# Performance work log

Hardware: AMD Instinct MI355X
Metric: run time of the kernel (lower is better)

## Reference

```python
import jax, jax.numpy as jnp
import numpy as np

N_NODES = 50000
N_EDGES = 800000
NODE_IN = 5
EDGE_IN = 1
HID = 64


def setup_inputs() -> dict:
    key = jax.random.key(0)
    ks = jax.random.split(key, 16)
    x = jax.random.normal(ks[0], (N_NODES, NODE_IN), dtype=jnp.float32)
    edge_index = jax.random.randint(ks[1], (2, N_EDGES), 0, N_NODES, dtype=jnp.int32)
    edge_attr = jax.random.normal(ks[2], (N_EDGES, EDGE_IN), dtype=jnp.float32)
    def lin(k, fan_in, fan_out):
        b = 1.0 / np.sqrt(fan_in)
        k1, k2 = jax.random.split(k)
        W = jax.random.uniform(k1, (fan_in, fan_out), minval=-b, maxval=b, dtype=jnp.float32)
        bi = jax.random.uniform(k2, (fan_out,), minval=-b, maxval=b, dtype=jnp.float32)
        return W, bi
    W_ne, b_ne = lin(ks[3], NODE_IN, HID)
    W_ee, b_ee = lin(ks[4], EDGE_IN, HID)
    W_gcn, b_gcn = lin(ks[5], HID, HID)   # PyG GCNConv: lin (no bias) + separate bias
    W1, b1 = lin(ks[6], 3 * HID, HID)
    W2, b2 = lin(ks[7], HID, 1)
    return {"x": x, "edge_index": edge_index, "edge_attr": edge_attr,
            "W_ne": W_ne, "b_ne": b_ne, "W_ee": W_ee, "b_ee": b_ee,
            "W_gcn": W_gcn, "b_gcn": b_gcn, "W1": W1, "b1": b1, "W2": W2, "b2": b2}


def gcn_conv(h, edge_index, W, b):
    # PyG GCNConv: add self-loops, symmetric norm D^-1/2 (A+I) D^-1/2, linear, scatter-add.
    N = h.shape[0]
    src, dst = edge_index[0], edge_index[1]
    loops = jnp.arange(N, dtype=src.dtype)
    row = jnp.concatenate([src, loops])  # message sources
    col = jnp.concatenate([dst, loops])  # message targets
    deg = jax.ops.segment_sum(jnp.ones(col.shape[0], h.dtype), col, num_segments=N)
    dinv = jnp.where(deg > 0, jax.lax.rsqrt(deg), 0.0)
    norm = dinv[row] * dinv[col]          # [E+N]
    ht = h @ W                            # [N, HID]
    msg = ht[row] * norm[:, None]         # gather + scale
    return jax.ops.segment_sum(msg, col, num_segments=N) + b


def reference(x, edge_index, edge_attr, W_ne, b_ne, W_ee, b_ee, W_gcn, b_gcn, W1, b1, W2, b2):
    h = jax.nn.relu(x @ W_ne + b_ne)                    # node encoder
    ef = jax.nn.relu(edge_attr @ W_ee + b_ee)           # edge encoder
    h = gcn_conv(h, edge_index, W_gcn, b_gcn)           # GCN layer
    src, dst = edge_index[0], edge_index[1]
    edge_input = jnp.concatenate([h[src], h[dst], ef], axis=1)  # [E, 3*HID]
    out = jax.nn.relu(edge_input @ W1 + b1) @ W2 + b2   # edge MLP -> [E, 1]
    return out.reshape(-1)
```

## Files before the change

### kernel.cpp

```cpp
#include <hip/hip_runtime.h>

#define NN 50000
#define NE 800000
#define H  64
#define NBKT 196
#define BCAP 8192
#define BIN_CHUNK 2048
#define NBIN (NE + BIN_CHUNK - 1) / BIN_CHUNK
#define CT4N (65 * 37)

typedef __attribute__((ext_vector_type(8))) short bf16x8;
typedef __attribute__((ext_vector_type(4))) float f32x4;

__device__ __forceinline__ unsigned short f2bf(float f) {
  unsigned int u = __builtin_bit_cast(unsigned int, f);
  u += 0x7FFFu + ((u >> 16) & 1u);
  return (unsigned short)(u >> 16);
}
__device__ __forceinline__ float bf2f(unsigned short u) {
  unsigned int v = ((unsigned int)u) << 16;
  return __builtin_bit_cast(float, v);
}

__global__ __launch_bounds__(256) void k_bin(
    const int* __restrict__ ei, unsigned int* __restrict__ gbin,
    int* __restrict__ gcur,
    const float* __restrict__ W1, const float* __restrict__ b1,
    const float* __restrict__ W_ee, const float* __restrict__ b_ee,
    float* __restrict__ thrS, float* __restrict__ cT,
    unsigned short* __restrict__ w1f) {
  const int t = threadIdx.x;

  if (blockIdx.x == NBIN + 1) {
    const int ln = t & 63, q = t >> 6;
    const int l15_ = ln & 15, l4_ = ln >> 4;
#pragma unroll
    for (int f = 0; f < 4; ++f) {
      const int idx = q * 4 + f;
      const int g = idx >> 3;
      const int ct = (idx >> 1) & 3;
      const int c = idx & 1;
#pragma unroll
      for (int j = 0; j < 8; ++j) {
        const int k = g * 64 + c * 32 + l4_ * 8 + j;
        const int hcol = ct * 16 + l15_;
        w1f[(idx * 64 + ln) * 8 + j] = f2bf(W1[k * H + hcol]);
      }
    }
    return;
  }

  if (blockIdx.x == NBIN) {
    __shared__ float swee[64], sbee[64], sth[64];
    __shared__ int skx[64];
    if (t < 64) {
      const float w = W_ee[t], b = b_ee[t];
      swee[t] = w; sbee[t] = b;
      sth[t] = (w != 0.f) ? (-b / w) : __builtin_inff();
      skx[t] = t;
    }
    __syncthreads();
    for (int sz = 2; sz <= 64; sz <<= 1)
      for (int st = sz >> 1; st > 0; st >>= 1) {
        if (t < 64) {
          const int p = t ^ st;
          if (p > t) {
            const bool up = ((t & sz) == 0);
            const float a = sth[t], bb = sth[p];
            if (up ? (a > bb) : (a < bb)) {
              const int ka = skx[t];
              sth[t] = bb; sth[p] = a;
              skx[t] = skx[p]; skx[p] = ka;
            }
          }
        }
        __syncthreads();
      }
    if (t < 64) {
      const int h = t;
      const int l4h = h >> 4, rh = (h & 15) >> 1, sub = h & 1;
      float c1 = 0.f, c0 = b1[h];
      for (int k = 0; k < 64; ++k) {
        const float w = swee[k], b = sbee[k];
        if (w < 0.f || (w == 0.f && b > 0.f)) {
          const float wv1 = W1[(128 + k) * H + h];
          c1 = fmaf(w, wv1, c1);
          c0 = fmaf(b, wv1, c0);
        }
      }
      {
        float* base = cT + (size_t)(0 * 37 + l4h * 9 + rh) * 4;
        base[2 * sub] = c1; base[2 * sub + 1] = c0;
      }
      for (int iv = 1; iv <= 64; ++iv) {
        const int ks = skx[iv - 1];
        const float w = swee[ks];
        const float s = (w > 0.f) ? 1.f : -1.f;
        const float wv1 = W1[(128 + ks) * H + h];
        c1 = fmaf(s * w, wv1, c1);
        c0 = fmaf(s * sbee[ks], wv1, c0);
        float* base = cT + (size_t)(iv * 37 + l4h * 9 + rh) * 4;
        base[2 * sub] = c1; base[2 * sub + 1] = c0;
      }
      thrS[h] = sth[h];
    }
    return;
  }

  __shared__ int hist[NBKT], base[NBKT];
  if (t < NBKT) hist[t] = 0;
  __syncthreads();

  const int e0 = blockIdx.x * BIN_CHUNK;
  int srcv[8], dstv[8], loff[8];
#pragma unroll
  for (int j = 0; j < 8; ++j) {
    const int e = e0 + j * 256 + t;
    if (e < NE) {
      srcv[j] = ei[e];
      dstv[j] = ei[NE + e];
      loff[j] = atomicAdd(&hist[dstv[j] >> 8], 1);
    } else dstv[j] = -1;
  }
  __syncthreads();
  if (t < NBKT) base[t] = atomicAdd(&gcur[t], hist[t]);
  __syncthreads();
#pragma unroll
  for (int j = 0; j < 8; ++j) {
    if (dstv[j] >= 0) {
      const int b = dstv[j] >> 8;
      const int pos = base[b] + loff[j];
      if (pos < BCAP)
        gbin[(size_t)b * BCAP + pos] =
            ((unsigned int)srcv[j] << 8) | (unsigned int)(dstv[j] & 255);
    }
  }
}

__global__ __launch_bounds__(256) void k_pass2(const unsigned int* __restrict__ gbin,
                                               const int* __restrict__ gcur,
                                               unsigned short* __restrict__ gcsr,
                                               int2* __restrict__ rowrange,
                                               float* __restrict__ dinv) {
  __shared__ int hist[256], cur[256], sc[256];
  __shared__ unsigned short lcsr[BCAP];
  const int b = blockIdx.x, t = threadIdx.x;
  const int sz = min(gcur[b], BCAP);
  hist[t] = 0;
  __syncthreads();

  const unsigned int* bb = gbin + (size_t)b * BCAP;
  unsigned int ent[32];
#pragma unroll
  for (int k = 0; k < 32; ++k) {
    const int i = t + k * 256;
    if (i < sz) {
      ent[k] = bb[i];
      atomicAdd(&hist[ent[k] & 255], 1);
    }
  }
  __syncthreads();

  int v = hist[t];
  const int cnt = v;
  sc[t] = v;
  __syncthreads();
#pragma unroll
  for (int off = 1; off < 256; off <<= 1) {
    const int o = (t >= off) ? sc[t - off] : 0;
    __syncthreads();
    v += o;
    sc[t] = v;
    __syncthreads();
  }
  const int ex = v - cnt;
  cur[t] = ex;
  const int d = b * 256 + t;
  if (d < NN) {
    const int beg = b * BCAP + ex;
    rowrange[d] = make_int2(beg, beg + cnt);
    dinv[d] = rsqrtf((float)(cnt + 1));
  }
  __syncthreads();

#pragma unroll
  for (int k = 0; k < 32; ++k) {
    const int i = t + k * 256;
    if (i < sz) {
      const unsigned int en = ent[k];
      const int off = atomicAdd(&cur[en & 255], 1);
      lcsr[off] = (unsigned short)(en >> 8);
    }
  }
  __syncthreads();
  for (int i = t; i < sz; i += 256) gcsr[(size_t)b * BCAP + i] = lcsr[i];
}

__global__ __launch_bounds__(256) void k_node(
    const float* __restrict__ x, const float* __restrict__ W_ne,
    const float* __restrict__ b_ne, const float* __restrict__ W_gcn,
    const float* __restrict__ dinv, unsigned short* __restrict__ htb) {
  __shared__ float sh[4][H];
  const int lane = threadIdx.x & 63;
  const int wv   = threadIdx.x >> 6;
  const int n    = blockIdx.x * 4 + wv;

  float acc = b_ne[lane];
#pragma unroll
  for (int k = 0; k < 5; ++k) acc = fmaf(x[n * 5 + k], W_ne[k * H + lane], acc);
  acc = fmaxf(acc, 0.0f);
  sh[wv][lane] = acc;
  __syncthreads();

  float hv = 0.0f;
#pragma unroll 8
  for (int k = 0; k < H; ++k) hv = fmaf(sh[wv][k], W_gcn[k * H + lane], hv);

  htb[(size_t)n * H + lane] = f2bf(hv * dinv[n]);
}

__global__ __launch_bounds__(256) void k_gather_uv(
    const int2* __restrict__ rowrange, const unsigned short* __restrict__ gcsr,
    const unsigned short* __restrict__ htb, const float* __restrict__ dinv,
    const float* __restrict__ b_gcn, const unsigned short* __restrict__ w1f,
    unsigned short* __restrict__ u, unsigned short* __restrict__ v) {
  __shared__ unsigned short shg[16 * 64];
  const int lane = threadIdx.x & 63;
  const int wv   = threadIdx.x >> 6;
  const int n0   = blockIdx.x * 16;
  const float bg = b_gcn[lane];

#pragma unroll 1
  for (int q = 0; q < 4; ++q) {
    const int nl = wv * 4 + q;
    const int n  = n0 + nl;
    const int2 rr = rowrange[n];
    float sum = bf2f(htb[(size_t)n * H + lane]);
    int i = rr.x;
#pragma unroll 1
    for (; i + 8 <= rr.y; i += 8) {
      const int s0 = gcsr[i],     s1 = gcsr[i + 1];
      const int s2 = gcsr[i + 2], s3 = gcsr[i + 3];
      const int s4 = gcsr[i + 4], s5 = gcsr[i + 5];
      const int s6 = gcsr[i + 6], s7 = gcsr[i + 7];
      const float v0 = bf2f(htb[(size_t)s0 * H + lane]);
      const float v1 = bf2f(htb[(size_t)s1 * H + lane]);
      const float v2 = bf2f(htb[(size_t)s2 * H + lane]);
      const float v3 = bf2f(htb[(size_t)s3 * H + lane]);
      const float v4 = bf2f(htb[(size_t)s4 * H + lane]);
      const float v5 = bf2f(htb[(size_t)s5 * H + lane]);
      const float v6 = bf2f(htb[(size_t)s6 * H + lane]);
      const float v7 = bf2f(htb[(size_t)s7 * H + lane]);
      sum += ((v0 + v1) + (v2 + v3)) + ((v4 + v5) + (v6 + v7));
    }
#pragma unroll 1
    for (; i < rr.y; ++i) sum += bf2f(htb[(size_t)gcsr[i] * H + lane]);

    const float hgv = fmaf(dinv[n], sum, bg);
    shg[((nl * 128 + lane * 2) ^ ((nl & 7) << 4)) >> 1] = f2bf(hgv);
  }
  __syncthreads();

  const int l15 = lane & 15, l4 = lane >> 4;
  const bf16x8 a0 = *(const bf16x8*)(shg + (((l15 * 128 + l4 * 16) ^ ((l15 & 7) << 4)) >> 1));
  const bf16x8 a1 = *(const bf16x8*)(shg + (((l15 * 128 + 64 + l4 * 16) ^ ((l15 & 7) << 4)) >> 1));

  const int ct = wv;
  const bf16x8 bu0 = *(const bf16x8*)(w1f + ((ct * 2 + 0) * 64 + lane) * 8);
  const bf16x8 bu1 = *(const bf16x8*)(w1f + ((ct * 2 + 1) * 64 + lane) * 8);
  const bf16x8 bv0 = *(const bf16x8*)(w1f + ((8 + ct * 2 + 0) * 64 + lane) * 8);
  const bf16x8 bv1 = *(const bf16x8*)(w1f + ((8 + ct * 2 + 1) * 64 + lane) * 8);

  f32x4 au = (f32x4)(0.f), av = (f32x4)(0.f);
  au = __builtin_amdgcn_mfma_f32_16x16x32_bf16(a0, bu0, au, 0, 0, 0);
  au = __builtin_amdgcn_mfma_f32_16x16x32_bf16(a1, bu1, au, 0, 0, 0);
  av = __builtin_amdgcn_mfma_f32_16x16x32_bf16(a0, bv0, av, 0, 0, 0);
  av = __builtin_amdgcn_mfma_f32_16x16x32_bf16(a1, bv1, av, 0, 0, 0);

#pragma unroll
  for (int r = 0; r < 4; ++r) {
    const size_t idx = (size_t)(n0 + l4 * 4 + r) * H + ct * 16 + l15;
    u[idx] = f2bf(au[r]);
    v[idx] = f2bf(av[r]);
  }
}

__device__ __forceinline__ int find_iv(const float* __restrict__ sThr, float ea) {
  int iv = 0;
#pragma unroll
  for (int st = 64; st >= 1; st >>= 1) {
    const int nc = iv + st;
    if (nc <= 64 && sThr[nc - 1] <= ea) iv = nc;
  }
  return iv;
}

__device__ __forceinline__ void edge_compute(
    float ea, uint4 U0, uint4 U1, uint4 V0, uint4 V1,
    const float* __restrict__ sThr, const float4* __restrict__ sCT4,
    const float* __restrict__ w2v, int l4, int lane, float b2v,
    float* __restrict__ out, int obase) {
  const int iv = find_iv(sThr, ea);
  const float4* cp = sCT4 + iv * 37 + l4 * 9;
  const unsigned int ud[8] = {U0.x, U0.y, U0.z, U0.w, U1.x, U1.y, U1.z, U1.w};
  const unsigned int vd[8] = {V0.x, V0.y, V0.z, V0.w, V1.x, V1.y, V1.z, V1.w};
  float p = 0.f;
#pragma unroll
  for (int r = 0; r < 8; ++r) {
    const float4 cc = cp[r];
    const float ulo = __builtin_bit_cast(float, ud[r] << 16);
    const float uhi = __builtin_bit_cast(float, ud[r] & 0xFFFF0000u);
    const float vlo = __builtin_bit_cast(float, vd[r] << 16);
    const float vhi = __builtin_bit_cast(float, vd[r] & 0xFFFF0000u);
    const float z0 = ulo + vlo + fmaf(ea, cc.x, cc.y);
    const float z1 = uhi + vhi + fmaf(ea, cc.z, cc.w);
    p = fmaf(fmaxf(z0, 0.f), w2v[2 * r], p);
    p = fmaf(fmaxf(z1, 0.f), w2v[2 * r + 1], p);
  }
  p += __shfl_xor(p, 16);
  p += __shfl_xor(p, 32);
  if (lane < 16) out[obase + lane] = p + b2v;
}

#define ET 5
__global__ __launch_bounds__(512) void k_edge(
    const int* __restrict__ ei, const float* __restrict__ eattr,
    const unsigned short* __restrict__ u, const unsigned short* __restrict__ v,
    const float* __restrict__ thrS, const float* __restrict__ cT,
    const float* __restrict__ W2, const float* __restrict__ b2,
    float* __restrict__ out) {
  __shared__ float sThr[64];
  __shared__ float4 sCT4[CT4N];

  const int t = threadIdx.x;
  if (t < 64) sThr[t] = thrS[t];
  {
    const float4* g = (const float4*)cT;
    for (int i = t; i < CT4N; i += 512) sCT4[i] = g[i];
  }
  __syncthreads();

  const int lane = t & 63;
  const int wv   = t >> 6;
  const int l15  = lane & 15, l4 = lane >> 4;
  const float b2v = b2[0];

  float w2v[16];
#pragma unroll
  for (int j = 0; j < 16; ++j) w2v[j] = W2[l4 * 16 + j];

  const int tile0 = (blockIdx.x * 8 + wv) * ET;
  int srcA[ET], dstA[ET];
  float eaA[ET];
#pragma unroll
  for (int tt = 0; tt < ET; ++tt) {
    srcA[tt] = ei[(tile0 + tt) * 16 + l15];
    dstA[tt] = ei[NE + (tile0 + tt) * 16 + l15];
    eaA[tt]  = eattr[(tile0 + tt) * 16 + l15];
  }

  uint4 Au0, Au1, Av0, Av1, Bu0, Bu1, Bv0, Bv1;

#define LOADUV(U0, U1, V0, V1, tt) {                               \
    const unsigned short* up = u + (size_t)srcA[tt] * H + l4 * 16; \
    const unsigned short* vp = v + (size_t)dstA[tt] * H + l4 * 16; \
    U0 = *(const uint4*)(up); U1 = *(const uint4*)(up + 8);        \
    V0 = *(const uint4*)(vp); V1 = *(const uint4*)(vp + 8); }

  LOADUV(Au0, Au1, Av0, Av1, 0);
  LOADUV(Bu0, Bu1, Bv0, Bv1, 1);
  edge_compute(eaA[0], Au0, Au1, Av0, Av1, sThr, sCT4, w2v, l4, lane, b2v, out, (tile0 + 0) * 16);
  LOADUV(Au0, Au1, Av0, Av1, 2);
  edge_compute(eaA[1], Bu0, Bu1, Bv0, Bv1, sThr, sCT4, w2v, l4, lane, b2v, out, (tile0 + 1) * 16);
  LOADUV(Bu0, Bu1, Bv0, Bv1, 3);
  edge_compute(eaA[2], Au0, Au1, Av0, Av1, sThr, sCT4, w2v, l4, lane, b2v, out, (tile0 + 2) * 16);
  LOADUV(Au0, Au1, Av0, Av1, 4);
  edge_compute(eaA[3], Bu0, Bu1, Bv0, Bv1, sThr, sCT4, w2v, l4, lane, b2v, out, (tile0 + 3) * 16);
  edge_compute(eaA[4], Au0, Au1, Av0, Av1, sThr, sCT4, w2v, l4, lane, b2v, out, (tile0 + 4) * 16);
#undef LOADUV
}

extern "C" void kernel_launch(void* const* d_in, const int* in_sizes, int n_in,
                              void* d_out, int out_size, void* d_ws, size_t ws_size,
                              hipStream_t stream) {
  const float* x     = (const float*)d_in[0];
  const int*   ei    = (const int*)d_in[1];
  const float* eattr = (const float*)d_in[2];
  const float* W_ne  = (const float*)d_in[3];
  const float* b_ne  = (const float*)d_in[4];
  const float* W_ee  = (const float*)d_in[5];
  const float* b_ee  = (const float*)d_in[6];
  const float* W_gcn = (const float*)d_in[7];
  const float* b_gcn = (const float*)d_in[8];
  const float* W1    = (const float*)d_in[9];
  const float* b1    = (const float*)d_in[10];
  const float* W2    = (const float*)d_in[11];
  const float* b2    = (const float*)d_in[12];
  float* out = (float*)d_out;

  char* ws = (char*)d_ws;
  unsigned short* htb = (unsigned short*)(ws + 0);
  unsigned short* uT  = (unsigned short*)(ws + 6400000);
  unsigned int*   gbin = (unsigned int*)(ws + 12800000);
  unsigned short* vT  = (unsigned short*)(ws + 12800000);
  unsigned short* gcsr = (unsigned short*)(ws + 19222528);
  int2*  rowrange = (int2*)(ws + 22433792);
  float* dinv    = (float*)(ws + 22833792);
  int*   gcur    = (int*)(ws + 23033792);
  float* thrS    = (float*)(ws + 23034592);
  float* cT      = (float*)(ws + 23034848);
  unsigned short* w1f = (unsigned short*)(ws + 23073328);

  hipMemsetAsync(gcur, 0, NBKT * sizeof(int), stream);
  k_bin<<<NBIN + 2, 256, 0, stream>>>(ei, gbin, gcur, W1, b1, W_ee, b_ee, thrS, cT, w1f);
  k_pass2<<<NBKT, 256, 0, stream>>>(gbin, gcur, gcsr, rowrange, dinv);
  k_node<<<NN / 4, 256, 0, stream>>>(x, W_ne, b_ne, W_gcn, dinv, htb);
  k_gather_uv<<<NN / 16, 256, 0, stream>>>(rowrange, gcsr, htb, dinv, b_gcn, w1f, uT, vT);
  k_edge<<<NE / (8 * ET * 16), 512, 0, stream>>>(ei, eattr, uT, vT, thrS, cT, W2, b2, out);
}
```

Baseline: 148.7 us.

## Vectorize bin loads and CSR copy, stage W1 in LDS, halve edge grid

Several unrelated changes. The binning kernel now has each thread load 8 contiguous edges with int4 loads instead of strided scalar loads. The CSR writeback copies 16 bytes at a time, and the cT precompute block stages the edge rows of W1 in shared memory instead of reading them from global. The edge kernel launches 625 blocks that each process two chunks, which amortises the per-block LDS table load but halves the number of resident blocks.

Measured after the change: 143.4 us, median of 2. 1.04x faster.

```diff
diff --git a/kernel.cpp b/kernel.cpp
--- a/kernel.cpp
+++ b/kernel.cpp
@@ -6,8 +6,10 @@
 #define NBKT 196
 #define BCAP 8192
 #define BIN_CHUNK 2048
-#define NBIN (NE + BIN_CHUNK - 1) / BIN_CHUNK
+#define NBIN ((NE + BIN_CHUNK - 1) / BIN_CHUNK)
 #define CT4N (65 * 37)
+#define ET 5
+#define ECHUNK 2
 
 typedef __attribute__((ext_vector_type(8))) short bf16x8;
 typedef __attribute__((ext_vector_type(4))) float f32x4;
@@ -51,8 +53,13 @@
   }
 
   if (blockIdx.x == NBIN) {
+    __shared__ float sW1[64][65];
     __shared__ float swee[64], sbee[64], sth[64];
     __shared__ int skx[64];
+    for (int i = t; i < 64 * 64; i += 256) {
+      const int k = i >> 6, h = i & 63;
+      sW1[k][h] = W1[(128 + k) * H + h];
+    }
     if (t < 64) {
       const float w = W_ee[t], b = b_ee[t];
       swee[t] = w; sbee[t] = b;
@@ -83,7 +90,7 @@
       for (int k = 0; k < 64; ++k) {
         const float w = swee[k], b = sbee[k];
         if (w < 0.f || (w == 0.f && b > 0.f)) {
-          const float wv1 = W1[(128 + k) * H + h];
+          const float wv1 = sW1[k][h];
           c1 = fmaf(w, wv1, c1);
           c0 = fmaf(b, wv1, c0);
         }
@@ -96,7 +103,7 @@
         const int ks = skx[iv - 1];
         const float w = swee[ks];
         const float s = (w > 0.f) ? 1.f : -1.f;
-        const float wv1 = W1[(128 + ks) * H + h];
+        const float wv1 = sW1[ks][h];
         c1 = fmaf(s * w, wv1, c1);
         c0 = fmaf(s * sbee[ks], wv1, c0);
         float* base = cT + (size_t)(iv * 37 + l4h * 9 + rh) * 4;
@@ -113,14 +120,28 @@
 
   const int e0 = blockIdx.x * BIN_CHUNK;
   int srcv[8], dstv[8], loff[8];
-#pragma unroll
-  for (int j = 0; j < 8; ++j) {
-    const int e = e0 + j * 256 + t;
-    if (e < NE) {
-      srcv[j] = ei[e];
-      dstv[j] = ei[NE + e];
-      loff[j] = atomicAdd(&hist[dstv[j] >> 8], 1);
-    } else dstv[j] = -1;
+  if (e0 + BIN_CHUNK <= NE) {
+    const int eb = e0 + t * 8;
+    const int4 sa = *(const int4*)(ei + eb);
+    const int4 sb = *(const int4*)(ei + eb + 4);
+    const int4 da = *(const int4*)(ei + NE + eb);
+    const int4 db = *(const int4*)(ei + NE + eb + 4);
+    srcv[0] = sa.x; srcv[1] = sa.y; srcv[2] = sa.z; srcv[3] = sa.w;
+    srcv[4] = sb.x; srcv[5] = sb.y; srcv[6] = sb.z; srcv[7] = sb.w;
+    dstv[0] = da.x; dstv[1] = da.y; dstv[2] = da.z; dstv[3] = da.w;
+    dstv[4] = db.x; dstv[5] = db.y; dstv[6] = db.z; dstv[7] = db.w;
+#pragma unroll
+    for (int j = 0; j < 8; ++j) loff[j] = atomicAdd(&hist[dstv[j] >> 8], 1);
+  } else {
+#pragma unroll
+    for (int j = 0; j < 8; ++j) {
+      const int e = e0 + t * 8 + j;
+      if (e < NE) {
+        srcv[j] = ei[e];
+        dstv[j] = ei[NE + e];
+        loff[j] = atomicAdd(&hist[dstv[j] >> 8], 1);
+      } else dstv[j] = -1;
+    }
   }
   __syncthreads();
   if (t < NBKT) base[t] = atomicAdd(&gcur[t], hist[t]);
@@ -193,7 +214,12 @@
     }
   }
   __syncthreads();
-  for (int i = t; i < sz; i += 256) gcsr[(size_t)b * BCAP + i] = lcsr[i];
+  {
+    const int n4 = (sz + 7) >> 3;
+    uint4* gdst = (uint4*)(gcsr + (size_t)b * BCAP);
+    const uint4* lsrc = (const uint4*)lcsr;
+    for (int i = t; i < n4; i += 256) gdst[i] = lsrc[i];
+  }
 }
 
 __global__ __launch_bounds__(256) void k_node(
@@ -322,7 +348,6 @@
   if (lane < 16) out[obase + lane] = p + b2v;
 }
 
-#define ET 5
 __global__ __launch_bounds__(512) void k_edge(
     const int* __restrict__ ei, const float* __restrict__ eattr,
     const unsigned short* __restrict__ u, const unsigned short* __restrict__ v,
@@ -349,17 +374,19 @@
 #pragma unroll
   for (int j = 0; j < 16; ++j) w2v[j] = W2[l4 * 16 + j];
 
-  const int tile0 = (blockIdx.x * 8 + wv) * ET;
-  int srcA[ET], dstA[ET];
-  float eaA[ET];
-#pragma unroll
-  for (int tt = 0; tt < ET; ++tt) {
-    srcA[tt] = ei[(tile0 + tt) * 16 + l15];
-    dstA[tt] = ei[NE + (tile0 + tt) * 16 + l15];
-    eaA[tt]  = eattr[(tile0 + tt) * 16 + l15];
-  }
-
-  uint4 Au0, Au1, Av0, Av1, Bu0, Bu1, Bv0, Bv1;
+#pragma unroll 1
+  for (int c = 0; c < ECHUNK; ++c) {
+    const int tile0 = (((c * 625) + blockIdx.x) * 8 + wv) * ET;
+    int srcA[ET], dstA[ET];
+    float eaA[ET];
+#pragma unroll
+    for (int tt = 0; tt < ET; ++tt) {
+      srcA[tt] = ei[(tile0 + tt) * 16 + l15];
+      dstA[tt] = ei[NE + (tile0 + tt) * 16 + l15];
+      eaA[tt]  = eattr[(tile0 + tt) * 16 + l15];
+    }
+
+    uint4 Au0, Au1, Av0, Av1, Bu0, Bu1, Bv0, Bv1;
 
 #define LOADUV(U0, U1, V0, V1, tt) {                               \
     const unsigned short* up = u + (size_t)srcA[tt] * H + l4 * 16; \
@@ -367,17 +394,18 @@
     U0 = *(const uint4*)(up); U1 = *(const uint4*)(up + 8);        \
     V0 = *(const uint4*)(vp); V1 = *(const uint4*)(vp + 8); }
 
-  LOADUV(Au0, Au1, Av0, Av1, 0);
-  LOADUV(Bu0, Bu1, Bv0, Bv1, 1);
-  edge_compute(eaA[0], Au0, Au1, Av0, Av1, sThr, sCT4, w2v, l4, lane, b2v, out, (tile0 + 0) * 16);
-  LOADUV(Au0, Au1, Av0, Av1, 2);
-  edge_compute(eaA[1], Bu0, Bu1, Bv0, Bv1, sThr, sCT4, w2v, l4, lane, b2v, out, (tile0 + 1) * 16);
-  LOADUV(Bu0, Bu1, Bv0, Bv1, 3);
-  edge_compute(eaA[2], Au0, Au1, Av0, Av1, sThr, sCT4, w2v, l4, lane, b2v, out, (tile0 + 2) * 16);
-  LOADUV(Au0, Au1, Av0, Av1, 4);
-  edge_compute(eaA[3], Bu0, Bu1, Bv0, Bv1, sThr, sCT4, w2v, l4, lane, b2v, out, (tile0 + 3) * 16);
-  edge_compute(eaA[4], Au0, Au1, Av0, Av1, sThr, sCT4, w2v, l4, lane, b2v, out, (tile0 + 4) * 16);
+    LOADUV(Au0, Au1, Av0, Av1, 0);
+    LOADUV(Bu0, Bu1, Bv0, Bv1, 1);
+    edge_compute(eaA[0], Au0, Au1, Av0, Av1, sThr, sCT4, w2v, l4, lane, b2v, out, (tile0 + 0) * 16);
+    LOADUV(Au0, Au1, Av0, Av1, 2);
+    edge_compute(eaA[1], Bu0, Bu1, Bv0, Bv1, sThr, sCT4, w2v, l4, lane, b2v, out, (tile0 + 1) * 16);
+    LOADUV(Bu0, Bu1, Bv0, Bv1, 3);
+    edge_compute(eaA[2], Au0, Au1, Av0, Av1, sThr, sCT4, w2v, l4, lane, b2v, out, (tile0 + 2) * 16);
+    LOADUV(Au0, Au1, Av0, Av1, 4);
+    edge_compute(eaA[3], Bu0, Bu1, Bv0, Bv1, sThr, sCT4, w2v, l4, lane, b2v, out, (tile0 + 3) * 16);
+    edge_compute(eaA[4], Au0, Au1, Av0, Av1, sThr, sCT4, w2v, l4, lane, b2v, out, (tile0 + 4) * 16);
 #undef LOADUV
+  }
 }
 
 extern "C" void kernel_launch(void* const* d_in, const int* in_sizes, int n_in,
@@ -416,5 +444,5 @@
   k_pass2<<<NBKT, 256, 0, stream>>>(gbin, gcur, gcsr, rowrange, dinv);
   k_node<<<NN / 4, 256, 0, stream>>>(x, W_ne, b_ne, W_gcn, dinv, htb);
   k_gather_uv<<<NN / 16, 256, 0, stream>>>(rowrange, gcsr, htb, dinv, b_gcn, w1f, uT, vT);
-  k_edge<<<NE / (8 * ET * 16), 512, 0, stream>>>(ei, eattr, uT, vT, thrS, cT, W2, b2, out);
-}
+  k_edge<<<625, 512, 0, stream>>>(ei, eattr, uT, vT, thrS, cT, W2, b2, out);
+}
```
